# Performance work log

Hardware: AMD Instinct MI355X
Metric: run time of the kernel (lower is better)

## Reference

```python
import jax, jax.numpy as jnp
import numpy as np

BETA = 0.25  # commitment weight per level (vqconfig default)
EPS = 1e-12  # F.normalize eps


def setup_inputs() -> dict:
    key = jax.random.key(0)
    k1, k2 = jax.random.split(key)
    z = jax.random.normal(k1, (4, 256, 32, 32), dtype=jnp.float32)
    cb = jax.random.normal(k2, (4, 4096, 256), dtype=jnp.float32)
    # embeddings are row-normalized at init in the torch module
    cb = cb / jnp.maximum(jnp.linalg.norm(cb, axis=-1, keepdims=True), EPS)
    return {"z": z, "codebooks": cb}


def _nearest_code(r_flat, embed):
    """use_znorm=True path: cosine-similarity nearest neighbor.
    r_flat: (N, C), embed: (K, C) -> idx: (N,) int32"""
    rn = r_flat / jnp.maximum(jnp.linalg.norm(r_flat, axis=1, keepdims=True), EPS)
    en = embed / jnp.maximum(jnp.linalg.norm(embed, axis=1, keepdims=True), EPS)
    sim = jnp.einsum('nc,kc->nk', rn, en)  # (N, K)
    return jnp.argmax(sim, axis=1)


def reference(z, codebooks):
    """Residual VQ over L codebooks (eval mode: no EMA / kmeans init).
    z: (B, C, H, W); codebooks: (L, K, C).
    Returns (z_q_st (B,C,H,W), indices (L,B,H,W), qloss scalar)."""
    B, C, H, W = z.shape
    L = codebooks.shape[0]
    z_flat = z.transpose(0, 2, 3, 1).reshape(-1, C)  # (N, C)
    residual = z_flat
    q_sum = jnp.zeros_like(z_flat)
    qloss = jnp.zeros((), dtype=z.dtype)
    indices = []
    for l in range(L):  # small fixed level loop with sequential data dependency
        E = codebooks[l]
        idx = _nearest_code(residual, E)          # (N,)
        z_q = E[idx]                              # gather (N, C)
        q_sum = q_sum + z_q
        qloss = qloss + BETA * jnp.mean((jax.lax.stop_gradient(z_q) - residual) ** 2)
        residual = residual - jax.lax.stop_gradient(z_q)
        indices.append(idx.reshape(B, H, W))
    q = q_sum.reshape(B, H, W, C).transpose(0, 3, 1, 2)
    z_q_st = z + jax.lax.stop_gradient(q - z)     # straight-through estimator
    return z_q_st, jnp.stack(indices, axis=0), qloss
```

## Files before the change

kernel.cpp:

```cpp
#include <hip/hip_runtime.h>


#define OFF_AS   0
#define OFF_BS   524288
#define OFF_R    2621440
#define OFF_INV  3670016
#define OFF_PV   3686400
#define OFF_RN   3817472
#define OFF_CNT  3821568
#define OFF_CAND 3825664
#define OFF_CVAL 4874240
#define OFF_SSQ  5922816

#define BETA 0.25f
#define EPSN 1e-12f
#define CAP 256
#define SLC 16
#define OVF (1 << 20)
#define MARGIN 0.012f
#define NEGINF -3.0e38f

typedef __attribute__((ext_vector_type(8))) short short8;
typedef __attribute__((ext_vector_type(4))) short short4v;
typedef __attribute__((ext_vector_type(4))) float f32x4;

__device__ __forceinline__ unsigned short f2bf(float x) {
  unsigned u = __float_as_uint(x);
  unsigned r = (u + 0x7fffu + ((u >> 16) & 1u)) >> 16;
  return (unsigned short)r;
}

__device__ __forceinline__ void gload16(const void* g, void* s) {
  __builtin_amdgcn_global_load_lds(
      (const __attribute__((address_space(1))) unsigned int*)g,
      (__attribute__((address_space(3))) unsigned int*)s, 16, 0, 0);
}

__global__ __launch_bounds__(256) void k_prep(const float* __restrict__ z,
                                              const float* __restrict__ cb,
                                              float* __restrict__ r,
                                              unsigned short* __restrict__ AS,
                                              float* __restrict__ rnorm,
                                              int* __restrict__ cnt,
                                              float* __restrict__ inv,
                                              unsigned short* __restrict__ BS) {
  __shared__ __align__(16) char psm[9472];
  int tid = threadIdx.x;
  int w = tid >> 6, lane = tid & 63;
  if (blockIdx.x < 2048) {
    float (*t)[260] = (float(*)[260])psm;
    float* sinvs = (float*)(psm + 8320);
    int r0 = blockIdx.x * 8;
#pragma unroll
    for (int p = 0; p < 2; ++p) {
      int idx = p * 1024 + tid * 4;
      float4 v = *(const float4*)(cb + (size_t)r0 * 256 + idx);
      int row = idx >> 8, c = idx & 255;
      *(float4*)&t[row][c] = v;
    }
    __syncthreads();
#pragma unroll
    for (int rr = 0; rr < 2; ++rr) {
      int row = w * 2 + rr;
      float4 v = *(const float4*)&t[row][lane * 4];
      float s = v.x * v.x + v.y * v.y + v.z * v.z + v.w * v.w;
#pragma unroll
      for (int off = 32; off; off >>= 1) s += __shfl_xor(s, off);
      if (lane == 0) sinvs[row] = 1.0f / fmaxf(sqrtf(s), EPSN);
    }
    __syncthreads();
    if (tid < 8) inv[r0 + tid] = sinvs[tid];
#pragma unroll
    for (int p = 0; p < 2; ++p) {
      int idx = p * 1024 + tid * 4;
      int row = idx >> 8, c = idx & 255;
      float sc = sinvs[row];
      short4v s4;
      s4[0] = (short)f2bf(t[row][c + 0] * sc);
      s4[1] = (short)f2bf(t[row][c + 1] * sc);
      s4[2] = (short)f2bf(t[row][c + 2] * sc);
      s4[3] = (short)f2bf(t[row][c + 3] * sc);
      *(short4v*)(BS + (size_t)r0 * 256 + idx) = s4;
    }
  } else {
    float (*t)[9] = (float(*)[9])psm;
    float* wpart = (float*)(psm + 9216);
    int n0 = (blockIdx.x - 2048) * 8;
    int b = n0 >> 10, hw0 = n0 & 1023;
#pragma unroll
    for (int p = 0; p < 8; ++p) {
      int c = p * 32 + (tid >> 3), h = tid & 7;
      t[c][h] = z[((b * 256 + c) << 10) + hw0 + h];
    }
    __syncthreads();
#pragma unroll
    for (int h = 0; h < 8; ++h) {
      float v = t[tid][h];
      float s = v * v;
#pragma unroll
      for (int off = 32; off; off >>= 1) s += __shfl_xor(s, off);
      if (lane == 0) wpart[w * 8 + h] = s;
    }
    __syncthreads();
    if (tid < 8) {
      float tot = (wpart[0 * 8 + tid] + wpart[1 * 8 + tid]) +
                  (wpart[2 * 8 + tid] + wpart[3 * 8 + tid]);
      rnorm[n0 + tid] = sqrtf(tot);
      cnt[n0 + tid] = 0;
    }
#pragma unroll
    for (int h = 0; h < 8; ++h) {
      float v = t[tid][h];
      r[(n0 + h) * 256 + tid] = v;
      AS[(n0 + h) * 256 + tid] = f2bf(v);
    }
  }
}

__global__ __launch_bounds__(256) void k_gemm_argmax(
    const unsigned short* __restrict__ AS, const unsigned short* __restrict__ BS,
    float* __restrict__ pval, const float* __restrict__ rnorm,
    int* __restrict__ cnt, int* __restrict__ cand, float* __restrict__ cval) {
  __shared__ __align__(16) char sm[32768];
  unsigned short* lA = (unsigned short*)sm;
  unsigned short* lB = (unsigned short*)(sm + 16384);
  float* sv    = (float*)sm;
  float* scomb = (float*)(sm + 1024);
  float* rn_s  = (float*)(sm + 1536);
  int*   lcnt  = (int*)(sm + 2048);
  int*   lck   = (int*)(sm + 2560);
  float* lcv   = (float*)(sm + 10752);

  int bid = blockIdx.x;
  int wg = (bid & 7) * 128 + (bid >> 3);
  int bm = wg >> 5, bn = wg & 31;
  int mbase = bm * 128, nbase = bn * 128;
  int tid = threadIdx.x;
  int wid = tid >> 6, ln = tid & 63;
  int wr = wid >> 1, wc = wid & 1;
  int grp = ln >> 4, li = ln & 15;

  f32x4 acc[4][4];
#pragma unroll
  for (int i = 0; i < 4; ++i)
#pragma unroll
    for (int j = 0; j < 4; ++j) acc[i][j] = (f32x4){0.f, 0.f, 0.f, 0.f};

  for (int ks = 0; ks < 4; ++ks) {
    __syncthreads();
    int k0 = ks * 64;
#pragma unroll
    for (int i = 0; i < 4; ++i) {
      int idx = i * 256 + tid;
      int row = idx >> 3, cc = idx & 7;
      int src = cc ^ (row & 7);
      gload16(AS + ((mbase + row) << 8) + k0 + src * 8, ((char*)lA) + idx * 16);
    }
#pragma unroll
    for (int i = 0; i < 4; ++i) {
      int idx = i * 256 + tid;
      int row = idx >> 3, cc = idx & 7;
      int src = cc ^ (row & 7);
      gload16(BS + ((nbase + row) << 8) + k0 + src * 8, ((char*)lB) + idx * 16);
    }
    __syncthreads();
#pragma unroll
    for (int kk = 0; kk < 2; ++kk) {
      short8 b[4];
#pragma unroll
      for (int ni = 0; ni < 4; ++ni) {
        int row = wc * 64 + ni * 16 + li;
        int cc = kk * 4 + grp;
        b[ni] = *(const short8*)(((const char*)lB) + row * 128 + (cc ^ (row & 7)) * 16);
      }
#pragma unroll
      for (int mi = 0; mi < 4; ++mi) {
        int row = wr * 64 + mi * 16 + li;
        int cc = kk * 4 + grp;
        short8 a = *(const short8*)(((const char*)lA) + row * 128 + (cc ^ (row & 7)) * 16);
#pragma unroll
        for (int ni = 0; ni < 4; ++ni)
          acc[mi][ni] = __builtin_amdgcn_mfma_f32_16x16x32_bf16(a, b[ni], acc[mi][ni], 0, 0, 0);
      }
    }
  }

  float redv[4][4];
#pragma unroll
  for (int mi = 0; mi < 4; ++mi) {
#pragma unroll
    for (int reg = 0; reg < 4; ++reg) {
      float v = acc[mi][0][reg];
#pragma unroll
      for (int ni = 1; ni < 4; ++ni) v = fmaxf(v, acc[mi][ni][reg]);
#pragma unroll
      for (int off = 1; off < 16; off <<= 1) v = fmaxf(v, __shfl_xor(v, off));
      redv[mi][reg] = v;
    }
  }
  __syncthreads();
#pragma unroll
  for (int mi = 0; mi < 4; ++mi)
#pragma unroll
    for (int reg = 0; reg < 4; ++reg)
      if (li == 0) sv[(wr * 2 + wc) * 64 + mi * 16 + grp * 4 + reg] = redv[mi][reg];
  __syncthreads();
  if (tid < 128) {
    int wr2 = tid >> 6, r64 = tid & 63;
    float m = fmaxf(sv[(wr2 * 2 + 0) * 64 + r64], sv[(wr2 * 2 + 1) * 64 + r64]);
    int n = mbase + wr2 * 64 + r64;
    pval[n * 32 + bn] = m;
    scomb[wr2 * 64 + r64] = m;
    rn_s[wr2 * 64 + r64] = rnorm[n];
    lcnt[tid] = 0;
  }
  __syncthreads();
#pragma unroll
  for (int mi = 0; mi < 4; ++mi) {
#pragma unroll
    for (int reg = 0; reg < 4; ++reg) {
      int rl = mi * 16 + grp * 4 + reg;
      float thr = scomb[wr * 64 + rl] - MARGIN * rn_s[wr * 64 + rl];
      int rloc = wr * 64 + rl;
#pragma unroll
      for (int ni = 0; ni < 4; ++ni) {
        float v = acc[mi][ni][reg];
        if (v >= thr) {
          int pos = atomicAdd(&lcnt[rloc], 1);
          if (pos < SLC) {
            lck[rloc * SLC + pos] = nbase + wc * 64 + ni * 16 + li;
            lcv[rloc * SLC + pos] = v;
          }
        }
      }
    }
  }
  __syncthreads();
  if (tid < 128) {
    int rloc = tid;
    int n = mbase + rloc;
    int raw = lcnt[rloc];
    int lc = raw < SLC ? raw : SLC;
    int add = raw > SLC ? (lc + OVF) : lc;
    if (add > 0) {
      int base = atomicAdd(&cnt[n], add);
      for (int j = 0; j < lc; ++j) {
        int pos = base + j;
        if (pos < CAP) {
          cand[n * CAP + pos] = lck[rloc * SLC + j];
          cval[n * CAP + pos] = lcv[rloc * SLC + j];
        }
      }
    }
  }
}

__global__ __launch_bounds__(256) void k_refine_update(
    const float* __restrict__ cb, const float* __restrict__ inv,
    float* __restrict__ r, const float* __restrict__ pval,
    float* __restrict__ rnorm, int* __restrict__ cnt,
    const int* __restrict__ cand, const float* __restrict__ cval,
    unsigned short* __restrict__ AS, float* __restrict__ ssq,
    float* __restrict__ out_idx, int l) {
  __shared__ int lists[4][CAP];
  __shared__ int lcnts[4];
  int tid = threadIdx.x, w = tid >> 6, lane = tid & 63;
  int n = blockIdx.x * 4 + w;
  const float* cbl = cb + ((size_t)l << 20);
  const float* invl = inv + (l << 12);

  float4 rv4 = *(const float4*)(r + ((size_t)n << 8) + lane * 4);

  float v = (lane < 32) ? pval[n * 32 + lane] : NEGINF;
#pragma unroll
  for (int off = 16; off; off >>= 1) v = fmaxf(v, __shfl_xor(v, off));
  float gm = __shfl(v, 0);

  if (lane == 0) lcnts[w] = 0;
  int c = cnt[n];
  float bv = NEGINF; int bk = 0x7fffffff;

  if (c <= CAP) {
    float thr = gm - MARGIN * rnorm[n];
    for (int j = lane; j < c; j += 64) {
      if (cval[n * CAP + j] >= thr) {
        int p = atomicAdd(&lcnts[w], 1);
        lists[w][p] = cand[n * CAP + j];
      }
    }
    int m = lcnts[w];
    for (int j = 0; j < m; ++j) {
      int k = lists[w][j];
      float4 e4 = *(const float4*)(cbl + ((size_t)k << 8) + lane * 4);
      float p = rv4.x * e4.x + rv4.y * e4.y + rv4.z * e4.z + rv4.w * e4.w;
#pragma unroll
      for (int off = 32; off; off >>= 1) p += __shfl_xor(p, off);
      float s = p * invl[k];
      if (s > bv || (s == bv && k < bk)) { bv = s; bk = k; }
    }
  } else {
    for (int k = 0; k < 4096; ++k) {
      float4 e4 = *(const float4*)(cbl + ((size_t)k << 8) + lane * 4);
      float p = rv4.x * e4.x + rv4.y * e4.y + rv4.z * e4.z + rv4.w * e4.w;
#pragma unroll
      for (int off = 32; off; off >>= 1) p += __shfl_xor(p, off);
      float s = p * invl[k];
      if (s > bv || (s == bv && k < bk)) { bv = s; bk = k; }
    }
  }
  if (lane == 0) out_idx[(l << 12) + n] = (float)bk;

  float4 e4 = *(const float4*)(cbl + ((size_t)bk << 8) + lane * 4);
  float4 nv = {rv4.x - e4.x, rv4.y - e4.y, rv4.z - e4.z, rv4.w - e4.w};
  *(float4*)(r + ((size_t)n << 8) + lane * 4) = nv;
  if (l != 3) {
    short4v s4;
    s4[0] = (short)f2bf(nv.x); s4[1] = (short)f2bf(nv.y);
    s4[2] = (short)f2bf(nv.z); s4[3] = (short)f2bf(nv.w);
    *(short4v*)(AS + ((size_t)n << 8) + lane * 4) = s4;
  }
  float sq = nv.x * nv.x + nv.y * nv.y + nv.z * nv.z + nv.w * nv.w;
#pragma unroll
  for (int off = 32; off; off >>= 1) sq += __shfl_xor(sq, off);
  if (lane == 0) {
    ssq[(l << 12) + n] = sq;
    if (l != 3) { rnorm[n] = sqrtf(sq); cnt[n] = 0; }
  }
}

__global__ __launch_bounds__(256) void k_writeq_qloss(const float* __restrict__ z,
                                                      const float* __restrict__ r,
                                                      const float* __restrict__ ssq,
                                                      float* __restrict__ out) {
  int tid = threadIdx.x;
  if (blockIdx.x == 1024) {
    __shared__ float wsumq[4];
    float q = 0.f;
    for (int l = 0; l < 4; ++l) {
      float p = 0.f;
#pragma unroll
      for (int i = 0; i < 16; ++i) p += ssq[l * 4096 + i * 256 + tid];
      int lane = tid & 63, w = tid >> 6;
#pragma unroll
      for (int off = 32; off; off >>= 1) p += __shfl_xor(p, off);
      if (lane == 0) wsumq[w] = p;
      __syncthreads();
      float tot = (wsumq[0] + wsumq[1]) + (wsumq[2] + wsumq[3]);
      q += BETA * (tot * (1.0f / (4096.0f * 256.0f)));
      __syncthreads();
    }
    if (tid == 0) out[1048576 + 16384] = q;
    return;
  }
  __shared__ float t[32][33];
  int id = blockIdx.x;
  int b = id >> 8; int rem = id & 255; int ct = rem >> 5; int ht = rem & 31;
  int c0 = ct * 32, h0 = ht * 32;
  int col = tid & 31, row0 = tid >> 5;
#pragma unroll
  for (int p = 0; p < 4; ++p) {
    int row = row0 + p * 8;
    t[row][col] = r[(b * 1024 + h0 + row) * 256 + c0 + col];
  }
  __syncthreads();
#pragma unroll
  for (int p = 0; p < 4; ++p) {
    int row = row0 + p * 8;
    int o = ((b * 256 + c0 + row) << 10) + h0 + col;
    out[o] = z[o] - t[col][row];
  }
}

extern "C" void kernel_launch(void* const* d_in, const int* in_sizes, int n_in,
                              void* d_out, int out_size, void* d_ws, size_t ws_size,
                              hipStream_t stream) {
  const float* z  = (const float*)d_in[0];
  const float* cb = (const float*)d_in[1];
  float* out = (float*)d_out;
  float* ws  = (float*)d_ws;

  unsigned short* AS = (unsigned short*)(ws + OFF_AS);
  unsigned short* BS = (unsigned short*)(ws + OFF_BS);
  float* r     = ws + OFF_R;
  float* inv   = ws + OFF_INV;
  float* pval  = ws + OFF_PV;
  float* rnorm = ws + OFF_RN;
  int*   cnt   = (int*)(ws + OFF_CNT);
  int*   cand  = (int*)(ws + OFF_CAND);
  float* cval  = ws + OFF_CVAL;
  float* ssq   = ws + OFF_SSQ;

  k_prep<<<2560, 256, 0, stream>>>(z, cb, r, AS, rnorm, cnt, inv, BS);
  for (int l = 0; l < 4; ++l) {
    k_gemm_argmax<<<1024, 256, 0, stream>>>(AS, BS + (size_t)l * 4096 * 256,
                                            pval, rnorm, cnt, cand, cval);
    k_refine_update<<<1024, 256, 0, stream>>>(cb, inv, r, pval, rnorm, cnt,
                                              cand, cval, AS, ssq,
                                              out + 1048576, l);
  }
  k_writeq_qloss<<<1025, 256, 0, stream>>>(z, r, ssq, out);
}
```

Measured before the change: 164.6 us.

## Store candidates in fixed per-tile slots instead of atomic global lists

The GEMM kernel now writes each column tile's candidates into a fixed 16-entry slot per row, plus a byte count per tile, instead of appending to a shared per-row list through global atomics. This removes the per-row partial-max array and the counter reset. The refine kernel loads all slots with vector loads and derives the global max from the stored candidate values. Tile overflow, or more than 128 surviving candidates, falls back to a full scan of all 4096 codes. This removes global atomic contention and extra buffers, at the cost of a larger workspace and unconditional reads of all 512 slots per row.

```diff
diff --git a/kernel.cpp b/kernel.cpp
--- a/kernel.cpp
+++ b/kernel.cpp
@@ -5,18 +5,14 @@
 #define OFF_BS   524288
 #define OFF_R    2621440
 #define OFF_INV  3670016
-#define OFF_PV   3686400
-#define OFF_RN   3817472
-#define OFF_CNT  3821568
-#define OFF_CAND 3825664
-#define OFF_CVAL 4874240
-#define OFF_SSQ  5922816
+#define OFF_CSLC 3686400
+#define OFF_CAND 3719168
+#define OFF_CVAL 5816320
+#define OFF_SSQ  7913472
 
 #define BETA 0.25f
 #define EPSN 1e-12f
-#define CAP 256
 #define SLC 16
-#define OVF (1 << 20)
 #define MARGIN 0.012f
 #define NEGINF -3.0e38f
 
@@ -41,7 +37,6 @@
                                               float* __restrict__ r,
                                               unsigned short* __restrict__ AS,
                                               float* __restrict__ rnorm,
-                                              int* __restrict__ cnt,
                                               float* __restrict__ inv,
                                               unsigned short* __restrict__ BS) {
   __shared__ __align__(16) char psm[9472];
@@ -106,7 +101,6 @@
       float tot = (wpart[0 * 8 + tid] + wpart[1 * 8 + tid]) +
                   (wpart[2 * 8 + tid] + wpart[3 * 8 + tid]);
       rnorm[n0 + tid] = sqrtf(tot);
-      cnt[n0 + tid] = 0;
     }
 #pragma unroll
     for (int h = 0; h < 8; ++h) {
@@ -119,8 +113,8 @@
 
 __global__ __launch_bounds__(256) void k_gemm_argmax(
     const unsigned short* __restrict__ AS, const unsigned short* __restrict__ BS,
-    float* __restrict__ pval, const float* __restrict__ rnorm,
-    int* __restrict__ cnt, int* __restrict__ cand, float* __restrict__ cval) {
+    const float* __restrict__ rnorm, unsigned char* __restrict__ cslc,
+    int* __restrict__ cand, float* __restrict__ cval) {
   __shared__ __align__(16) char sm[32768];
   unsigned short* lA = (unsigned short*)sm;
   unsigned short* lB = (unsigned short*)(sm + 16384);
@@ -209,7 +203,6 @@
     int wr2 = tid >> 6, r64 = tid & 63;
     float m = fmaxf(sv[(wr2 * 2 + 0) * 64 + r64], sv[(wr2 * 2 + 1) * 64 + r64]);
     int n = mbase + wr2 * 64 + r64;
-    pval[n * 32 + bn] = m;
     scomb[wr2 * 64 + r64] = m;
     rn_s[wr2 * 64 + r64] = rnorm[n];
     lcnt[tid] = 0;
@@ -241,28 +234,23 @@
     int n = mbase + rloc;
     int raw = lcnt[rloc];
     int lc = raw < SLC ? raw : SLC;
-    int add = raw > SLC ? (lc + OVF) : lc;
-    if (add > 0) {
-      int base = atomicAdd(&cnt[n], add);
-      for (int j = 0; j < lc; ++j) {
-        int pos = base + j;
-        if (pos < CAP) {
-          cand[n * CAP + pos] = lck[rloc * SLC + j];
-          cval[n * CAP + pos] = lcv[rloc * SLC + j];
-        }
-      }
+    cslc[(n << 5) + bn] = (unsigned char)(raw > SLC ? 255 : lc);
+    int base = (n << 9) + bn * SLC;
+    for (int j = 0; j < lc; ++j) {
+      cand[base + j] = lck[rloc * SLC + j];
+      cval[base + j] = lcv[rloc * SLC + j];
     }
   }
 }
 
 __global__ __launch_bounds__(256) void k_refine_update(
     const float* __restrict__ cb, const float* __restrict__ inv,
-    float* __restrict__ r, const float* __restrict__ pval,
-    float* __restrict__ rnorm, int* __restrict__ cnt,
+    float* __restrict__ r, float* __restrict__ rnorm,
+    const unsigned char* __restrict__ cslc,
     const int* __restrict__ cand, const float* __restrict__ cval,
     unsigned short* __restrict__ AS, float* __restrict__ ssq,
     float* __restrict__ out_idx, int l) {
-  __shared__ int lists[4][CAP];
+  __shared__ int lists[4][128];
   __shared__ int lcnts[4];
   int tid = threadIdx.x, w = tid >> 6, lane = tid & 63;
   int n = blockIdx.x * 4 + w;
@@ -271,34 +259,51 @@
 
   float4 rv4 = *(const float4*)(r + ((size_t)n << 8) + lane * 4);
 
-  float v = (lane < 32) ? pval[n * 32 + lane] : NEGINF;
-#pragma unroll
-  for (int off = 16; off; off >>= 1) v = fmaxf(v, __shfl_xor(v, off));
-  float gm = __shfl(v, 0);
-
-  if (lane == 0) lcnts[w] = 0;
-  int c = cnt[n];
+  int cnt_l = cslc[(n << 5) + (lane >> 1)];
+  bool ovf = __any(cnt_l == 255);
+  int sbase = (n << 9) + (lane >> 1) * 16 + (lane & 1) * 8;
+  int4 k0 = *(const int4*)(cand + sbase);
+  int4 k1 = *(const int4*)(cand + sbase + 4);
+  float4 v0 = *(const float4*)(cval + sbase);
+  float4 v1 = *(const float4*)(cval + sbase + 4);
+  int nvalid = cnt_l - ((lane & 1) << 3);
+  nvalid = nvalid < 0 ? 0 : (nvalid > 8 ? 8 : nvalid);
+  float vv[8] = {v0.x, v0.y, v0.z, v0.w, v1.x, v1.y, v1.z, v1.w};
+  int   kk[8] = {k0.x, k0.y, k0.z, k0.w, k1.x, k1.y, k1.z, k1.w};
+
+  float gm = NEGINF;
+#pragma unroll
+  for (int j = 0; j < 8; ++j) if (j < nvalid) gm = fmaxf(gm, vv[j]);
+#pragma unroll
+  for (int off = 32; off; off >>= 1) gm = fmaxf(gm, __shfl_xor(gm, off));
+
   float bv = NEGINF; int bk = 0x7fffffff;
-
-  if (c <= CAP) {
+  bool full = ovf;
+  if (!ovf) {
     float thr = gm - MARGIN * rnorm[n];
-    for (int j = lane; j < c; j += 64) {
-      if (cval[n * CAP + j] >= thr) {
+    if (lane == 0) lcnts[w] = 0;
+#pragma unroll
+    for (int j = 0; j < 8; ++j) {
+      if (j < nvalid && vv[j] >= thr) {
         int p = atomicAdd(&lcnts[w], 1);
-        lists[w][p] = cand[n * CAP + j];
+        if (p < 128) lists[w][p] = kk[j];
       }
     }
     int m = lcnts[w];
-    for (int j = 0; j < m; ++j) {
-      int k = lists[w][j];
-      float4 e4 = *(const float4*)(cbl + ((size_t)k << 8) + lane * 4);
-      float p = rv4.x * e4.x + rv4.y * e4.y + rv4.z * e4.z + rv4.w * e4.w;
-#pragma unroll
-      for (int off = 32; off; off >>= 1) p += __shfl_xor(p, off);
-      float s = p * invl[k];
-      if (s > bv || (s == bv && k < bk)) { bv = s; bk = k; }
-    }
-  } else {
+    if (m <= 128) {
+      for (int j = 0; j < m; ++j) {
+        int k = lists[w][j];
+        float4 e4 = *(const float4*)(cbl + ((size_t)k << 8) + lane * 4);
+        float p = rv4.x * e4.x + rv4.y * e4.y + rv4.z * e4.z + rv4.w * e4.w;
+#pragma unroll
+        for (int off = 32; off; off >>= 1) p += __shfl_xor(p, off);
+        float s = p * invl[k];
+        if (s > bv || (s == bv && k < bk)) { bv = s; bk = k; }
+      }
+    } else full = true;
+  }
+  if (full) {
+    bv = NEGINF; bk = 0x7fffffff;
     for (int k = 0; k < 4096; ++k) {
       float4 e4 = *(const float4*)(cbl + ((size_t)k << 8) + lane * 4);
       float p = rv4.x * e4.x + rv4.y * e4.y + rv4.z * e4.z + rv4.w * e4.w;
@@ -324,7 +329,7 @@
   for (int off = 32; off; off >>= 1) sq += __shfl_xor(sq, off);
   if (lane == 0) {
     ssq[(l << 12) + n] = sq;
-    if (l != 3) { rnorm[n] = sqrtf(sq); cnt[n] = 0; }
+    if (l != 3) rnorm[n] = sqrtf(sq);
   }
 }
 
@@ -383,18 +388,17 @@
   unsigned short* BS = (unsigned short*)(ws + OFF_BS);
   float* r     = ws + OFF_R;
   float* inv   = ws + OFF_INV;
-  float* pval  = ws + OFF_PV;
-  float* rnorm = ws + OFF_RN;
-  int*   cnt   = (int*)(ws + OFF_CNT);
+  unsigned char* cslc = (unsigned char*)(ws + OFF_CSLC);
   int*   cand  = (int*)(ws + OFF_CAND);
   float* cval  = ws + OFF_CVAL;
   float* ssq   = ws + OFF_SSQ;
-
-  k_prep<<<2560, 256, 0, stream>>>(z, cb, r, AS, rnorm, cnt, inv, BS);
+  float* rnorm = ws + OFF_SSQ + 16384;
+
+  k_prep<<<2560, 256, 0, stream>>>(z, cb, r, AS, rnorm, inv, BS);
   for (int l = 0; l < 4; ++l) {
     k_gemm_argmax<<<1024, 256, 0, stream>>>(AS, BS + (size_t)l * 4096 * 256,
-                                            pval, rnorm, cnt, cand, cval);
-    k_refine_update<<<1024, 256, 0, stream>>>(cb, inv, r, pval, rnorm, cnt,
+                                            rnorm, cslc, cand, cval);
+    k_refine_update<<<1024, 256, 0, stream>>>(cb, inv, r, rnorm, cslc,
                                               cand, cval, AS, ssq,
                                               out + 1048576, l);
   }
```

Result: no change. 166.3 us, median of 3 (+1.0%).
